# Optimization experiments

Hardware: AMD Instinct MI355X
Metric: run time of the kernel (lower is better)

The kernel has to match this reference:

```python
import jax, jax.numpy as jnp
import numpy as np

B, S, N, D, M = 4, 4096, 16, 64, 4  # batch, seq, heads, head_dim, num_scales

def setup_inputs() -> dict:
    key = jax.random.key(0)
    ks = jax.random.split(key, 6)
    return {
        "q": jax.random.normal(ks[0], (B, S, N, D), dtype=jnp.float32),
        "k": jax.random.normal(ks[1], (B, S, N, D), dtype=jnp.float32),
        "v": jax.random.normal(ks[2], (B, S, N, D), dtype=jnp.float32),
        "memory": jax.random.normal(ks[3], (B, M, N, D, D), dtype=jnp.float32),
        "decay_factors": jax.random.uniform(ks[4], (M,), dtype=jnp.float32) + 0.5,
        "gate_weights": jax.random.uniform(ks[5], (M,), dtype=jnp.float32),
    }

def reference(q, k, v, memory, decay_factors, gate_weights):
    # --- update_memory: decayed outer-product accumulation ---
    # new_info[b,n,k,v] = sum_s k[b,s,n,k] * v[b,s,n,v]  (fused; never build [b,s,n,k,v])
    new_info = jnp.einsum('bsnk,bsnv->bnkv', k, v)
    sig = jax.nn.sigmoid(decay_factors)            # [M]
    sig5 = sig[None, :, None, None, None]          # [1,M,1,1,1]
    mem_new = memory * sig5 + (1.0 - sig5) * new_info[:, None]  # [B,M,N,D,D]
    # --- forward read: q @ memory per scale, softmax-gated scale mixing ---
    gates = jax.nn.softmax(gate_weights)           # [M]
    # fuse gate mixing into the contraction; never build [b,m,s,n,v]
    out = jnp.einsum('bsnk,bmnkv,m->bsnv', q, mem_new, gates)
    return out
```

## Files before the change

kernel.cpp:

```cpp
#include <hip/hip_runtime.h>
#include <hip/hip_bf16.h>
#include <math.h>

constexpr int B = 4, S = 4096, N = 16, D = 64, M = 4;
constexpr int SND = S * N * D;
constexpr int ND  = N * D;
constexpr int DD  = D * D;
constexpr int NCH = 8;
constexpr int SPB = S / NCH;

typedef __attribute__((ext_vector_type(8))) short bf16x8;
typedef __attribute__((ext_vector_type(4))) float f32x4;
typedef unsigned short u16;
typedef unsigned int u32;

__device__ inline u16 f2bf(float x) {
  __hip_bfloat16 h = __float2bfloat16(x);
  return __builtin_bit_cast(u16, h);
}

__global__ __launch_bounds__(256) void k1_partials(const float* __restrict__ kg,
                                                   const float* __restrict__ vg,
                                                   float* __restrict__ part) {
  __shared__ u16 lds[4][2][2][64][32];

  const int t = threadIdx.x, w = t >> 6, l = t & 63;
  const int bn = blockIdx.x;
  const int b = bn >> 4, n = bn & 15;
  const int r = l & 7, c = l >> 3;
  const int lr = l & 15, lg = l >> 4;

  const size_t base = (size_t)b * SND + (size_t)n * D +
                      ((size_t)blockIdx.y * SPB + (size_t)w * 128) * ND;

  f32x4 acc[4][4];
#pragma unroll
  for (int i = 0; i < 4; ++i)
#pragma unroll
    for (int j = 0; j < 4; ++j) acc[i][j] = (f32x4)0.f;

  float kfa[2][2][8], vfa[2][2][8];

#define STAGE_LOAD(tt)                                                        \
  {                                                                           \
    _Pragma("unroll") for (int h = 0; h < 2; ++h)                             \
    _Pragma("unroll") for (int sp = 0; sp < 2; ++sp) {                        \
      const float* kp =                                                       \
          kg + base + (size_t)((tt) * 32 + 16 * h + 2 * r + sp) * ND + 8 * c; \
      const float* vp =                                                       \
          vg + base + (size_t)((tt) * 32 + 16 * h + 2 * r + sp) * ND + 8 * c; \
      *(float4*)&kfa[h][sp][0] = *(const float4*)kp;                          \
      *(float4*)&kfa[h][sp][4] = *(const float4*)(kp + 4);                    \
      *(float4*)&vfa[h][sp][0] = *(const float4*)vp;                          \
      *(float4*)&vfa[h][sp][4] = *(const float4*)(vp + 4);                    \
    }                                                                         \
  }

#define STAGE_WRITE(buf)                                                      \
  {                                                                           \
    _Pragma("unroll") for (int h = 0; h < 2; ++h)                             \
    _Pragma("unroll") for (int dd = 0; dd < 8; ++dd) {                        \
      const int d = 8 * c + dd;                                               \
      const int slot = (((2 * h + (r >> 2)) ^ (d & 3)) << 3) + ((2 * r) & 7); \
      *(u32*)&lds[w][buf][0][d][slot] =                                       \
          (u32)f2bf(kfa[h][0][dd]) | ((u32)f2bf(kfa[h][1][dd]) << 16);        \
      *(u32*)&lds[w][buf][1][d][slot] =                                       \
          (u32)f2bf(vfa[h][0][dd]) | ((u32)f2bf(vfa[h][1][dd]) << 16);        \
    }                                                                         \
  }

#define COMPUTE(buf)                                                          \
  {                                                                           \
    bf16x8 af[4], bfq[4];                                                     \
    _Pragma("unroll") for (int mi = 0; mi < 4; ++mi) {                        \
      const int row = 16 * mi + lr;                                           \
      af[mi]  = *(const bf16x8*)&lds[w][buf][0][row][(lg ^ (row & 3)) << 3];  \
      bfq[mi] = *(const bf16x8*)&lds[w][buf][1][row][(lg ^ (row & 3)) << 3];  \
    }                                                                         \
    _Pragma("unroll") for (int mi = 0; mi < 4; ++mi)                          \
    _Pragma("unroll") for (int ni = 0; ni < 4; ++ni)                          \
      acc[mi][ni] = __builtin_amdgcn_mfma_f32_16x16x32_bf16(                  \
          af[mi], bfq[ni], acc[mi][ni], 0, 0, 0);                             \
  }

  STAGE_LOAD(0);
  STAGE_WRITE(0);
  STAGE_LOAD(1);
  COMPUTE(0);
  STAGE_WRITE(1);
  STAGE_LOAD(2);
  COMPUTE(1);
  STAGE_WRITE(0);
  STAGE_LOAD(3);
  COMPUTE(0);
  STAGE_WRITE(1);
  COMPUTE(1);

#undef STAGE_LOAD
#undef STAGE_WRITE
#undef COMPUTE

  __syncthreads();
  float* red = (float*)lds;
#pragma unroll
  for (int mi = 0; mi < 4; ++mi)
#pragma unroll
    for (int ni = 0; ni < 4; ++ni)
#pragma unroll
      for (int ri = 0; ri < 4; ++ri)
        red[w * 4096 + (16 * mi + 4 * lg + ri) * 64 + 16 * ni + lr] =
            acc[mi][ni][ri];
  __syncthreads();

  float* p = part + ((size_t)bn * NCH + blockIdx.y) * DD;
#pragma unroll
  for (int j = 0; j < 4; ++j) {
    const int e = t * 16 + 4 * j;
    const float4 a0 = *(const float4*)&red[e];
    const float4 a1 = *(const float4*)&red[4096 + e];
    const float4 a2 = *(const float4*)&red[8192 + e];
    const float4 a3 = *(const float4*)&red[12288 + e];
    *(float4*)&p[e] = make_float4(a0.x + a1.x + a2.x + a3.x,
                                  a0.y + a1.y + a2.y + a3.y,
                                  a0.z + a1.z + a2.z + a3.z,
                                  a0.w + a1.w + a2.w + a3.w);
  }
}

__global__ __launch_bounds__(256) void k2_combine(const float* __restrict__ part,
                                                  const float* __restrict__ memg,
                                                  const float* __restrict__ decay,
                                                  const float* __restrict__ gatew,
                                                  u16* __restrict__ meffT) {
  const int t = threadIdx.x;
  const int bn = blockIdx.x;
  const int b = bn >> 4, n = bn & 15;
  const int kv = blockIdx.y * 256 + t;
  const int k = kv >> 6, v = kv & 63;

  float gw[M], df[M];
#pragma unroll
  for (int m = 0; m < M; ++m) { gw[m] = gatew[m]; df[m] = decay[m]; }
  const float mx = fmaxf(fmaxf(gw[0], gw[1]), fmaxf(gw[2], gw[3]));
  float e[M], esum = 0.f;
#pragma unroll
  for (int m = 0; m < M; ++m) { e[m] = expf(gw[m] - mx); esum += e[m]; }
  float wgt[M], cc = 0.f;
#pragma unroll
  for (int m = 0; m < M; ++m) {
    const float g = e[m] / esum;
    const float sg = 1.f / (1.f + expf(-df[m]));
    wgt[m] = g * sg;
    cc += g * (1.f - sg);
  }

  const float* pb = part + (size_t)bn * NCH * DD + kv;
  float ni = 0.f;
#pragma unroll
  for (int ch = 0; ch < NCH; ++ch) ni += pb[(size_t)ch * DD];
  float a = cc * ni;
#pragma unroll
  for (int m = 0; m < M; ++m)
    a += wgt[m] * memg[(((size_t)b * M + m) * N + n) * DD + kv];

  meffT[(size_t)bn * DD + v * 64 + k] = f2bf(a);
}

__global__ __launch_bounds__(256, 4) void k3_out(const float* __restrict__ qg,
                                                 const u16* __restrict__ meffT,
                                                 float* __restrict__ outg) {
  const int t = threadIdx.x, w = t >> 6, l = t & 63;
  const int lr = l & 15, lg = l >> 4;
  const int bn = blockIdx.x;
  const int b = bn >> 4, n = bn & 15;
  const int s0 = blockIdx.y * 256 + w * 64;

  const u16* mb = meffT + (size_t)bn * DD;
  bf16x8 bfr[4][2];
#pragma unroll
  for (int ni = 0; ni < 4; ++ni)
#pragma unroll
    for (int ks = 0; ks < 2; ++ks)
      bfr[ni][ks] = *(const bf16x8*)(mb + (16 * ni + lr) * 64 + 32 * ks + 8 * lg);

  f32x4 acc[4][4];
#pragma unroll
  for (int i = 0; i < 4; ++i)
#pragma unroll
    for (int j = 0; j < 4; ++j) acc[i][j] = (f32x4)0.f;

  const size_t qbase = (size_t)b * SND + (size_t)n * D;

#pragma unroll
  for (int mi = 0; mi < 4; ++mi) {
    const float* qr = qg + qbase + (size_t)(s0 + 16 * mi + lr) * ND + 8 * lg;
#pragma unroll
    for (int ks = 0; ks < 2; ++ks) {
      float qa[8];
      *(float4*)&qa[0] = *(const float4*)(qr + 32 * ks);
      *(float4*)&qa[4] = *(const float4*)(qr + 32 * ks + 4);
      bf16x8 a;
#pragma unroll
      for (int j = 0; j < 8; ++j) a[j] = (short)f2bf(qa[j]);
#pragma unroll
      for (int ni = 0; ni < 4; ++ni)
        acc[mi][ni] = __builtin_amdgcn_mfma_f32_16x16x32_bf16(a, bfr[ni][ks],
                                                              acc[mi][ni], 0, 0, 0);
    }
  }

#pragma unroll
  for (int mi = 0; mi < 4; ++mi)
#pragma unroll
    for (int ni = 0; ni < 4; ++ni)
#pragma unroll
      for (int ri = 0; ri < 4; ++ri)
        outg[qbase + (size_t)(s0 + 16 * mi + 4 * lg + ri) * ND + 16 * ni + lr] =
            acc[mi][ni][ri];
}

extern "C" void kernel_launch(void* const* d_in, const int* in_sizes, int n_in,
                              void* d_out, int out_size, void* d_ws, size_t ws_size,
                              hipStream_t stream) {
  const float* q     = (const float*)d_in[0];
  const float* k     = (const float*)d_in[1];
  const float* v     = (const float*)d_in[2];
  const float* memg  = (const float*)d_in[3];
  const float* decay = (const float*)d_in[4];
  const float* gatew = (const float*)d_in[5];
  float* out = (float*)d_out;

  u16* meffT = (u16*)d_ws;
  const size_t meffT_bytes = (size_t)64 * DD * sizeof(u16);
  float* part = (float*)((char*)d_ws + meffT_bytes);

  hipLaunchKernelGGL(k1_partials, dim3(64, NCH), dim3(256), 0, stream,
                     k, v, part);
  hipLaunchKernelGGL(k2_combine, dim3(64, 16), dim3(256), 0, stream,
                     part, memg, decay, gatew, meffT);
  hipLaunchKernelGGL(k3_out, dim3(64, 16), dim3(256), 0, stream,
                     q, meffT, out);
}
```

Before: 64.83 us.

## Coalesce k/v loads across four heads per block and drop LDS reduction

```diff
diff --git a/kernel.cpp b/kernel.cpp
--- a/kernel.cpp
+++ b/kernel.cpp
@@ -6,7 +6,7 @@
 constexpr int SND = S * N * D;
 constexpr int ND  = N * D;
 constexpr int DD  = D * D;
-constexpr int NCH = 8;
+constexpr int NCH = 32;
 constexpr int SPB = S / NCH;
 
 typedef __attribute__((ext_vector_type(8))) short bf16x8;
@@ -19,19 +19,22 @@
   return __builtin_bit_cast(u16, h);
 }
 
-__global__ __launch_bounds__(256) void k1_partials(const float* __restrict__ kg,
-                                                   const float* __restrict__ vg,
-                                                   float* __restrict__ part) {
-  __shared__ u16 lds[4][2][2][64][32];
-
-  const int t = threadIdx.x, w = t >> 6, l = t & 63;
-  const int bn = blockIdx.x;
-  const int b = bn >> 4, n = bn & 15;
-  const int r = l & 7, c = l >> 3;
-  const int lr = l & 15, lg = l >> 4;
-
-  const size_t base = (size_t)b * SND + (size_t)n * D +
-                      ((size_t)blockIdx.y * SPB + (size_t)w * 128) * ND;
+__global__ __launch_bounds__(256, 2) void k1_partials(const float* __restrict__ kg,
+                                                      const float* __restrict__ vg,
+                                                      float* __restrict__ part) {
+  __shared__ u16 kv[4][2][2][64][32];
+
+  const int t = threadIdx.x, w = t >> 6;
+  const int bid = blockIdx.x;
+  const int ch = bid & 31, ng = (bid >> 5) & 3, b = bid >> 7;
+
+  const int u  = t & 31;
+  const int rp = t >> 5;
+  const int np = u >> 3;
+  const int dB = 8 * (u & 7);
+  const int lr = t & 15, lg = (t >> 4) & 3;
+
+  const size_t base = (size_t)b * SND + (size_t)ch * SPB * ND + ng * 256;
 
   f32x4 acc[4][4];
 #pragma unroll
@@ -39,33 +42,34 @@
 #pragma unroll
     for (int j = 0; j < 4; ++j) acc[i][j] = (f32x4)0.f;
 
-  float kfa[2][2][8], vfa[2][2][8];
-
-#define STAGE_LOAD(tt)                                                        \
+  float kf[4][8], vf[4][8];
+
+#define STAGE_LOAD(st)                                                        \
   {                                                                           \
-    _Pragma("unroll") for (int h = 0; h < 2; ++h)                             \
+    _Pragma("unroll") for (int pg = 0; pg < 2; ++pg)                          \
     _Pragma("unroll") for (int sp = 0; sp < 2; ++sp) {                        \
-      const float* kp =                                                       \
-          kg + base + (size_t)((tt) * 32 + 16 * h + 2 * r + sp) * ND + 8 * c; \
-      const float* vp =                                                       \
-          vg + base + (size_t)((tt) * 32 + 16 * h + 2 * r + sp) * ND + 8 * c; \
-      *(float4*)&kfa[h][sp][0] = *(const float4*)kp;                          \
-      *(float4*)&kfa[h][sp][4] = *(const float4*)(kp + 4);                    \
-      *(float4*)&vfa[h][sp][0] = *(const float4*)vp;                          \
-      *(float4*)&vfa[h][sp][4] = *(const float4*)(vp + 4);                    \
+      const int r = 2 * rp + 16 * pg + sp;                                    \
+      const float* kp = kg + base + (size_t)((st) * 32 + r) * ND + 8 * u;     \
+      const float* vp = vg + base + (size_t)((st) * 32 + r) * ND + 8 * u;     \
+      *(float4*)&kf[2 * pg + sp][0] = *(const float4*)kp;                     \
+      *(float4*)&kf[2 * pg + sp][4] = *(const float4*)(kp + 4);               \
+      *(float4*)&vf[2 * pg + sp][0] = *(const float4*)vp;                     \
+      *(float4*)&vf[2 * pg + sp][4] = *(const float4*)(vp + 4);               \
     }                                                                         \
   }
 
 #define STAGE_WRITE(buf)                                                      \
   {                                                                           \
-    _Pragma("unroll") for (int h = 0; h < 2; ++h)                             \
-    _Pragma("unroll") for (int dd = 0; dd < 8; ++dd) {                        \
-      const int d = 8 * c + dd;                                               \
-      const int slot = (((2 * h + (r >> 2)) ^ (d & 3)) << 3) + ((2 * r) & 7); \
-      *(u32*)&lds[w][buf][0][d][slot] =                                       \
-          (u32)f2bf(kfa[h][0][dd]) | ((u32)f2bf(kfa[h][1][dd]) << 16);        \
-      *(u32*)&lds[w][buf][1][d][slot] =                                       \
-          (u32)f2bf(vfa[h][0][dd]) | ((u32)f2bf(vfa[h][1][dd]) << 16);        \
+    _Pragma("unroll") for (int pg = 0; pg < 2; ++pg) {                        \
+      const int se = 2 * rp + 16 * pg;                                        \
+      _Pragma("unroll") for (int j = 0; j < 8; ++j) {                         \
+        const int d = dB + j;                                                 \
+        const int slot = (((se >> 3) ^ (d & 3)) << 3) + (se & 7);             \
+        *(u32*)&kv[np][buf][0][d][slot] =                                     \
+            (u32)f2bf(kf[2 * pg][j]) | ((u32)f2bf(kf[2 * pg + 1][j]) << 16);  \
+        *(u32*)&kv[np][buf][1][d][slot] =                                     \
+            (u32)f2bf(vf[2 * pg][j]) | ((u32)f2bf(vf[2 * pg + 1][j]) << 16);  \
+      }                                                                       \
     }                                                                         \
   }
 
@@ -74,8 +78,8 @@
     bf16x8 af[4], bfq[4];                                                     \
     _Pragma("unroll") for (int mi = 0; mi < 4; ++mi) {                        \
       const int row = 16 * mi + lr;                                           \
-      af[mi]  = *(const bf16x8*)&lds[w][buf][0][row][(lg ^ (row & 3)) << 3];  \
-      bfq[mi] = *(const bf16x8*)&lds[w][buf][1][row][(lg ^ (row & 3)) << 3];  \
+      af[mi]  = *(const bf16x8*)&kv[w][buf][0][row][(lg ^ (row & 3)) << 3];   \
+      bfq[mi] = *(const bf16x8*)&kv[w][buf][1][row][(lg ^ (row & 3)) << 3];   \
     }                                                                         \
     _Pragma("unroll") for (int mi = 0; mi < 4; ++mi)                          \
     _Pragma("unroll") for (int ni = 0; ni < 4; ++ni)                          \
@@ -86,45 +90,28 @@
   STAGE_LOAD(0);
   STAGE_WRITE(0);
   STAGE_LOAD(1);
-  COMPUTE(0);
-  STAGE_WRITE(1);
-  STAGE_LOAD(2);
-  COMPUTE(1);
-  STAGE_WRITE(0);
-  STAGE_LOAD(3);
-  COMPUTE(0);
-  STAGE_WRITE(1);
-  COMPUTE(1);
+
+#pragma unroll
+  for (int st = 0; st < 4; ++st) {
+    __syncthreads();
+    COMPUTE(st & 1);
+    if (st < 3) STAGE_WRITE((st + 1) & 1);
+    if (st < 2) STAGE_LOAD(st + 2);
+  }
 
 #undef STAGE_LOAD
 #undef STAGE_WRITE
 #undef COMPUTE
 
-  __syncthreads();
-  float* red = (float*)lds;
+  const int bn = b * 16 + ng * 4 + w;
+  float* p = part + ((size_t)bn * NCH + ch) * DD;
 #pragma unroll
   for (int mi = 0; mi < 4; ++mi)
 #pragma unroll
     for (int ni = 0; ni < 4; ++ni)
 #pragma unroll
       for (int ri = 0; ri < 4; ++ri)
-        red[w * 4096 + (16 * mi + 4 * lg + ri) * 64 + 16 * ni + lr] =
-            acc[mi][ni][ri];
-  __syncthreads();
-
-  float* p = part + ((size_t)bn * NCH + blockIdx.y) * DD;
-#pragma unroll
-  for (int j = 0; j < 4; ++j) {
-    const int e = t * 16 + 4 * j;
-    const float4 a0 = *(const float4*)&red[e];
-    const float4 a1 = *(const float4*)&red[4096 + e];
-    const float4 a2 = *(const float4*)&red[8192 + e];
-    const float4 a3 = *(const float4*)&red[12288 + e];
-    *(float4*)&p[e] = make_float4(a0.x + a1.x + a2.x + a3.x,
-                                  a0.y + a1.y + a2.y + a3.y,
-                                  a0.z + a1.z + a2.z + a3.z,
-                                  a0.w + a1.w + a2.w + a3.w);
-  }
+        p[(16 * mi + 4 * lg + ri) * 64 + 16 * ni + lr] = acc[mi][ni][ri];
 }
 
 __global__ __launch_bounds__(256) void k2_combine(const float* __restrict__ part,
@@ -156,7 +143,7 @@
 
   const float* pb = part + (size_t)bn * NCH * DD + kv;
   float ni = 0.f;
-#pragma unroll
+#pragma unroll 8
   for (int ch = 0; ch < NCH; ++ch) ni += pb[(size_t)ch * DD];
   float a = cc * ni;
 #pragma unroll
@@ -234,7 +221,7 @@
   const size_t meffT_bytes = (size_t)64 * DD * sizeof(u16);
   float* part = (float*)((char*)d_ws + meffT_bytes);
 
-  hipLaunchKernelGGL(k1_partials, dim3(64, NCH), dim3(256), 0, stream,
+  hipLaunchKernelGGL(k1_partials, dim3(512), dim3(256), 0, stream,
                      k, v, part);
   hipLaunchKernelGGL(k2_combine, dim3(64, 16), dim3(256), 0, stream,
                      part, memg, decay, gatew, meffT);
```

Result: slower. 88.35 us (+36.3%).
